# Optimization experiments

Measured on AMD Instinct MI355X. Metric: run time of the kernel, lower is better.

Reference implementation:

```python
import jax, jax.numpy as jnp
import numpy as np

B, LP, LQ, D = 32, 2048, 512, 256

def setup_inputs() -> dict:
    key = jax.random.key(0)
    k1, k2, k3, k4 = jax.random.split(key, 4)
    x = jax.random.normal(k1, (B, LP, D), dtype=jnp.float32)
    y = jax.random.normal(k2, (B, LQ, D), dtype=jnp.float32)
    # nn.Linear(input_size, input_size): weight [D, D], bias [D]
    bound = 1.0 / np.sqrt(D)
    W = jax.random.uniform(k3, (D, D), minval=-bound, maxval=bound, dtype=jnp.float32)
    b = jax.random.uniform(k4, (D,), minval=-bound, maxval=bound, dtype=jnp.float32)
    return {"x": x, "y": y, "W": W, "b": b}

def reference(x, y, W, b):
    # shared linear + relu projection (torch Linear: x @ W.T + b)
    x_proj = jax.nn.relu(jnp.einsum('bpd,ed->bpe', x, W) + b)  # [B, LP, D]
    y_proj = jax.nn.relu(jnp.einsum('bqd,ed->bqe', y, W) + b)  # [B, LQ, D]
    # unscaled cross-attention scores
    scores = jnp.einsum('bpd,bqd->bpq', x_proj, y_proj)        # [B, LP, LQ]
    alpha = jax.nn.softmax(scores, axis=-1)
    # weighted sum over original (unprojected) y
    match_seq = jnp.einsum('bpq,bqd->bpd', alpha, y)           # [B, LP, D]
    return match_seq
```

## Files before the change

kernel.cpp:

```cpp
#include <hip/hip_runtime.h>
#include <stdint.h>

#define B_  32
#define LP_ 2048
#define LQ_ 512
#define D_  256

typedef __attribute__((ext_vector_type(8))) short short8;
typedef __attribute__((ext_vector_type(8))) _Float16 f16x8;
typedef __attribute__((ext_vector_type(4))) float f32x4;

__device__ __forceinline__ ushort f2h(float x) {
    union { _Float16 h; ushort u; } v;
    v.h = (_Float16)x;
    return v.u;
}
__device__ __forceinline__ void gl_lds16(const void* g, void* l) {
    __builtin_amdgcn_global_load_lds(
        (const __attribute__((address_space(1))) void*)g,
        (__attribute__((address_space(3))) void*)l, 16, 0, 0);
}


__global__ void k_prep(const float* __restrict__ W, const float* __restrict__ y,
                       ushort* __restrict__ Whf, ushort* __restrict__ yf) {
    __shared__ float t[32 * 260];
    if (blockIdx.x < 256) {
        int i = blockIdx.x * 256 + threadIdx.x;
        int e = i >> 8, k = i & 255;
        size_t off = (size_t)((k >> 5) * 16 + (e >> 4)) * 512 +
                     ((k >> 3) & 3) * 128 + (e & 15) * 8 + (k & 7);
        Whf[off] = f2h(W[i]);
        return;
    }
    int bid = blockIdx.x - 256;
    int b = bid >> 4, qc = bid & 15;
    int tid = threadIdx.x;
    int ql = tid >> 3;
    int d0 = (tid & 7) * 4;
#pragma unroll
    for (int p = 0; p < 8; p++) {
        int d = p * 32 + d0;
        float4 v = *(const float4*)(y + ((size_t)(b * LQ_ + qc * 32 + ql) * 256 + d));
        t[ql * 260 + d + 0] = v.x; t[ql * 260 + d + 1] = v.y;
        t[ql * 260 + d + 2] = v.z; t[ql * 260 + d + 3] = v.w;
    }
    __syncthreads();
    int w = tid >> 6, L = tid & 63, c = L & 15, quad = L >> 4;
#pragma unroll
    for (int ii = 0; ii < 4; ii++) {
        int nt = w * 4 + ii;
        short8 o;
#pragma unroll
        for (int j = 0; j < 8; j++)
            o[j] = (short)f2h(t[(quad * 8 + j) * 260 + nt * 16 + c]);
        *(short8*)(yf + ((size_t)(b * 256 + qc * 16 + nt) * 512 + L * 8)) = o;
    }
}

__global__ __launch_bounds__(256, 3) void k_proj(const float* __restrict__ y,
                                                 const ushort* __restrict__ Whf,
                                                 const float* __restrict__ bias,
                                                 ushort* __restrict__ Oy) {
    __shared__ __align__(16) ushort Ws[16704];
    const int tid  = threadIdx.x;
    const int w    = tid >> 6;
    const int L    = tid & 63;
    const int c    = L & 15;
    const int quad = L >> 4;
    const int row0 = blockIdx.x * 64 + w * 16;
    const int arow = row0 + c;

    f32x4 acc[16];
#pragma unroll
    for (int i = 0; i < 16; i++) acc[i] = (f32x4)0.f;

#define PSTAGE(kc, p)                                                          \
    {                                                                          \
        _Pragma("unroll")                                                      \
        for (int ii = 0; ii < 4; ii++) {                                       \
            int i = w * 4 + ii;                                                \
            gl_lds16(Whf + (size_t)(kc) * 8192 + i * 512 + L * 8,              \
                     (char*)Ws + (p) * 16384 + i * 1024);                      \
        }                                                                      \
    }

    PSTAGE(0, 0);
    float4 nx0 = *(const float4*)(y + (size_t)arow * 256 + quad * 8);
    float4 nx1 = *(const float4*)(y + (size_t)arow * 256 + quad * 8 + 4);

    for (int kc = 0; kc < 8; kc++) {
        __syncthreads();
        if (kc < 7) PSTAGE(kc + 1, (kc + 1) & 1);
        float4 cx0 = nx0, cx1 = nx1;
        if (kc < 7) {
            nx0 = *(const float4*)(y + (size_t)arow * 256 + (kc + 1) * 32 + quad * 8);
            nx1 = *(const float4*)(y + (size_t)arow * 256 + (kc + 1) * 32 + quad * 8 + 4);
        }
        float xs[8] = {cx0.x, cx0.y, cx0.z, cx0.w, cx1.x, cx1.y, cx1.z, cx1.w};
        f16x8 ah;
#pragma unroll
        for (int j = 0; j < 8; j++) ah[j] = (_Float16)xs[j];
        const ushort* buf = Ws + (kc & 1) * 8192;
#pragma unroll
        for (int nt = 0; nt < 16; nt++) {
            f16x8 bh = *(const f16x8*)(buf + nt * 512 + L * 8);
            acc[nt] = __builtin_amdgcn_mfma_f32_16x16x32_f16(ah, bh, acc[nt], 0, 0, 0);
        }
    }

    __syncthreads();
    float* tr = (float*)Ws + w * (16 * 130);
    const int rt_g = row0 >> 4;
#pragma unroll
    for (int half = 0; half < 2; half++) {
#pragma unroll
        for (int nt8 = 0; nt8 < 8; nt8++) {
            int nt = half * 8 + nt8;
            float bv = bias[nt * 16 + c];
#pragma unroll
            for (int r = 0; r < 4; r++)
                tr[(quad * 4 + r) * 130 + nt8 * 16 + c] = fmaxf(acc[nt][r] + bv, 0.f);
        }
#pragma unroll
        for (int ec4 = 0; ec4 < 4; ec4++) {
            int ec = half * 4 + ec4;
            short8 hh;
#pragma unroll
            for (int j = 0; j < 8; j++)
                hh[j] = (short)f2h(tr[c * 130 + ec4 * 32 + quad * 8 + j]);
            size_t blk = (size_t)(rt_g >> 5) * 256 + ec * 32 + (rt_g & 31);
            *(short8*)(Oy + blk * 512 + L * 8) = hh;
        }
    }
}

__global__ __launch_bounds__(256, 4) void k_attn(const float* __restrict__ x,
                                                 const ushort* __restrict__ Whf,
                                                 const float* __restrict__ bias,
                                                 const ushort* __restrict__ ypf,
                                                 const ushort* __restrict__ yf,
                                                 float* __restrict__ out) {
    __shared__ __align__(16) ushort lds[16384];
    const int tid  = threadIdx.x;
    const int w    = tid >> 6;
    const int L    = tid & 63;
    const int c    = L & 15;
    const int quad = L >> 4;

    const int bid = blockIdx.x;
    const int jj  = bid >> 3;
    const int b   = (bid & 7) * 4 + (jj >> 6);
    const int mt  = jj & 63;
    const int m0  = mt * 32;

#pragma unroll
    for (int ii = 0; ii < 4; ii++) {
        int unit = w * 4 + ii;
        int rs = unit >> 3, kc = unit & 7;
        const float* xs = x + ((size_t)(b * LP_ + m0 + rs * 16 + c)) * 256 + kc * 32 + quad * 8;
        float4 v0 = *(const float4*)xs;
        float4 v1 = *(const float4*)(xs + 4);
        f16x8 h;
        h[0] = (_Float16)v0.x; h[1] = (_Float16)v0.y;
        h[2] = (_Float16)v0.z; h[3] = (_Float16)v0.w;
        h[4] = (_Float16)v1.x; h[5] = (_Float16)v1.y;
        h[6] = (_Float16)v1.z; h[7] = (_Float16)v1.w;
        *(f16x8*)(lds + unit * 512 + L * 8) = h;
    }
    __syncthreads();

    {
        float bv[4];
#pragma unroll
        for (int ne = 0; ne < 4; ne++) bv[ne] = bias[(w * 4 + ne) * 16 + c];
        f32x4 pacc[2][4];
#pragma unroll
        for (int rs = 0; rs < 2; rs++)
#pragma unroll
            for (int ne = 0; ne < 4; ne++) pacc[rs][ne] = (f32x4)0.f;
        for (int kc = 0; kc < 8; kc++) {
            f16x8 ah0 = *(const f16x8*)(lds + kc * 512 + L * 8);
            f16x8 ah1 = *(const f16x8*)(lds + (8 + kc) * 512 + L * 8);
#pragma unroll
            for (int ne = 0; ne < 4; ne++) {
                f16x8 wb = *(const f16x8*)(Whf + ((size_t)(kc * 16 + w * 4 + ne)) * 512 + L * 8);
                pacc[0][ne] = __builtin_amdgcn_mfma_f32_16x16x32_f16(ah0, wb, pacc[0][ne], 0, 0, 0);
                pacc[1][ne] = __builtin_amdgcn_mfma_f32_16x16x32_f16(ah1, wb, pacc[1][ne], 0, 0, 0);
            }
        }
#pragma unroll
        for (int rs = 0; rs < 2; rs++)
#pragma unroll
            for (int ne = 0; ne < 4; ne++) {
#pragma unroll
                for (int r = 0; r < 4; r++) {
                    float v = fmaxf(pacc[rs][ne][r] + bv[ne], 0.f);
                    int off = 8192 + (rs * 8 + w * 2 + (ne >> 1)) * 512 +
                              ((ne & 1) * 2 + (c >> 3)) * 128 + (quad * 4 + r) * 8 + (c & 7);
                    lds[off] = f2h(v);
                }
            }
    }

    f32x4 sc[2][8];
#pragma unroll
    for (int rs = 0; rs < 2; rs++)
#pragma unroll
        for (int qt = 0; qt < 8; qt++) sc[rs][qt] = (f32x4)0.f;
    __syncthreads();

    const ushort* pf = lds + 8192;
    const ushort* yb = ypf + (size_t)b * 256 * 512;
    for (int kc = 0; kc < 8; kc++) {
        f16x8 ah0 = *(const f16x8*)(pf + kc * 512 + L * 8);
        f16x8 ah1 = *(const f16x8*)(pf + (8 + kc) * 512 + L * 8);
#pragma unroll
        for (int qt = 0; qt < 8; qt++) {
            f16x8 bh = *(const f16x8*)(yb + ((size_t)kc * 32 + w * 8 + qt) * 512 + L * 8);
            sc[0][qt] = __builtin_amdgcn_mfma_f32_16x16x32_f16(ah0, bh, sc[0][qt], 0, 0, 0);
            sc[1][qt] = __builtin_amdgcn_mfma_f32_16x16x32_f16(ah1, bh, sc[1][qt], 0, 0, 0);
        }
    }

    __syncthreads();
    float* red  = (float*)lds;
    float* red2 = red + 128;
    float inv[2][4];
#pragma unroll
    for (int rs = 0; rs < 2; rs++)
#pragma unroll
        for (int r = 0; r < 4; r++) {
            float pm = sc[rs][0][r];
#pragma unroll
            for (int qt = 1; qt < 8; qt++) pm = fmaxf(pm, sc[rs][qt][r]);
#pragma unroll
            for (int mask = 1; mask <= 8; mask <<= 1) pm = fmaxf(pm, __shfl_xor(pm, mask));
            if (c == 0) red[(rs * 16 + quad * 4 + r) * 4 + w] = pm;
        }
    __syncthreads();
#pragma unroll
    for (int rs = 0; rs < 2; rs++)
#pragma unroll
        for (int r = 0; r < 4; r++) {
            int row = rs * 16 + quad * 4 + r;
            float m = fmaxf(fmaxf(red[row * 4], red[row * 4 + 1]),
                            fmaxf(red[row * 4 + 2], red[row * 4 + 3]));
            float ps = 0.f;
#pragma unroll
            for (int qt = 0; qt < 8; qt++) {
                float e = __expf(sc[rs][qt][r] - m);
                sc[rs][qt][r] = e;
                ps += e;
            }
#pragma unroll
            for (int mask = 1; mask <= 8; mask <<= 1) ps += __shfl_xor(ps, mask);
            if (c == 0) red2[row * 4 + w] = ps;
        }
    __syncthreads();
#pragma unroll
    for (int rs = 0; rs < 2; rs++)
#pragma unroll
        for (int r = 0; r < 4; r++) {
            int row = rs * 16 + quad * 4 + r;
            inv[rs][r] = 1.f / (red2[row * 4] + red2[row * 4 + 1] +
                                red2[row * 4 + 2] + red2[row * 4 + 3]);
        }
    __syncthreads();

#pragma unroll
    for (int rs = 0; rs < 2; rs++)
#pragma unroll
        for (int r = 0; r < 4; r++) {
            int m_loc = rs * 16 + quad * 4 + r;
            int swz = m_loc & 7;
            float iv = inv[rs][r];
#pragma unroll
            for (int qt = 0; qt < 8; qt++) {
                int q = w * 128 + qt * 16 + c;
                lds[m_loc * 512 + (((q >> 3) ^ swz) << 3) + (c & 7)] = f2h(sc[rs][qt][r] * iv);
            }
        }
    __syncthreads();

    f32x4 o[2][4];
#pragma unroll
    for (int rs = 0; rs < 2; rs++)
#pragma unroll
        for (int dt = 0; dt < 4; dt++) o[rs][dt] = (f32x4)0.f;
    const int dh = w;
    const int swzA = c & 7;
    for (int kcq = 0; kcq < 16; kcq++) {
        int chunk = kcq * 4 + quad;
        f16x8 af0 = *(const f16x8*)(lds + c * 512 + ((chunk ^ swzA) << 3));
        f16x8 af1 = *(const f16x8*)(lds + (16 + c) * 512 + ((chunk ^ swzA) << 3));
        const ushort* ybf = yf + ((size_t)(b * 256 + kcq * 16 + dh * 4)) * 512;
#pragma unroll
        for (int dt = 0; dt < 4; dt++) {
            f16x8 bfr = *(const f16x8*)(ybf + dt * 512 + L * 8);
            o[0][dt] = __builtin_amdgcn_mfma_f32_16x16x32_f16(af0, bfr, o[0][dt], 0, 0, 0);
            o[1][dt] = __builtin_amdgcn_mfma_f32_16x16x32_f16(af1, bfr, o[1][dt], 0, 0, 0);
        }
    }

#pragma unroll
    for (int rs = 0; rs < 2; rs++)
#pragma unroll
        for (int dt = 0; dt < 4; dt++)
#pragma unroll
            for (int r = 0; r < 4; r++) {
                int row = rs * 16 + quad * 4 + r;
                out[(size_t)(b * LP_ + m0 + row) * 256 + dh * 64 + dt * 16 + c] =
                    o[rs][dt][r];
            }
}

extern "C" void kernel_launch(void* const* d_in, const int* in_sizes, int n_in,
                              void* d_out, int out_size, void* d_ws, size_t ws_size,
                              hipStream_t stream) {
    const float* x    = (const float*)d_in[0];
    const float* y    = (const float*)d_in[1];
    const float* W    = (const float*)d_in[2];
    const float* bias = (const float*)d_in[3];
    float* out = (float*)d_out;

    char* ws = (char*)d_ws;
    size_t off = 0;
    ushort* Whf = (ushort*)(ws + off); off += (size_t)D_ * D_ * 2;
    ushort* yfb = (ushort*)(ws + off); off += (size_t)B_ * D_ * LQ_ * 2;
    ushort* ypf = (ushort*)(ws + off); off += (size_t)B_ * LQ_ * D_ * 2;

    k_prep<<<768, 256, 0, stream>>>(W, y, Whf, yfb);
    k_proj<<<256, 256, 0, stream>>>(y, Whf, bias, ypf);
    k_attn<<<B_ * 64, 256, 0, stream>>>(x, Whf, bias, ypf, yfb, out);
}
```

Before: 196.4 us.

## Double-buffer W and projected-y fragments in LDS via async global-to-LDS loads

Weight fragments for the projection GEMM and projected-y fragments for the score GEMM are now staged into double-buffered LDS with global_load_lds. The next chunk is prefetched while MFMAs run on the current one, instead of each wave loading directly from global memory inside the MFMA loop. The score phase is also repartitioned so each wave owns one 16-row slab and half the q columns, which simplifies the softmax reductions to two partials per row. This raises LDS use to 48KB per block, which may cut occupancy below the 4 blocks per CU in launch bounds, and adds many more barriers.

```diff
diff --git a/kernel.cpp b/kernel.cpp
--- a/kernel.cpp
+++ b/kernel.cpp
@@ -141,7 +141,7 @@
                                                  const ushort* __restrict__ ypf,
                                                  const ushort* __restrict__ yf,
                                                  float* __restrict__ out) {
-    __shared__ __align__(16) ushort lds[16384];
+    __shared__ __align__(16) ushort lds[24576];
     const int tid  = threadIdx.x;
     const int w    = tid >> 6;
     const int L    = tid & 63;
@@ -168,7 +168,10 @@
         h[6] = (_Float16)v1.z; h[7] = (_Float16)v1.w;
         *(f16x8*)(lds + unit * 512 + L * 8) = h;
     }
-    __syncthreads();
+#pragma unroll
+    for (int ii = 0; ii < 4; ii++)
+        gl_lds16(Whf + (size_t)(w * 4 + ii) * 512 + L * 8,
+                 (char*)lds + 16384 + (w * 4 + ii) * 1024);
 
     {
         float bv[4];
@@ -179,16 +182,30 @@
         for (int rs = 0; rs < 2; rs++)
 #pragma unroll
             for (int ne = 0; ne < 4; ne++) pacc[rs][ne] = (f32x4)0.f;
+#pragma unroll
         for (int kc = 0; kc < 8; kc++) {
+            __syncthreads();
+            if (kc < 7) {
+#pragma unroll
+                for (int ii = 0; ii < 4; ii++)
+                    gl_lds16(Whf + (size_t)((kc + 1) * 16 + w * 4 + ii) * 512 + L * 8,
+                             (char*)lds + 16384 + ((kc + 1) & 1) * 16384 + (w * 4 + ii) * 1024);
+            }
             f16x8 ah0 = *(const f16x8*)(lds + kc * 512 + L * 8);
             f16x8 ah1 = *(const f16x8*)(lds + (8 + kc) * 512 + L * 8);
+            const ushort* wbuf = lds + 8192 + (kc & 1) * 8192;
 #pragma unroll
             for (int ne = 0; ne < 4; ne++) {
-                f16x8 wb = *(const f16x8*)(Whf + ((size_t)(kc * 16 + w * 4 + ne)) * 512 + L * 8);
+                f16x8 wb = *(const f16x8*)(wbuf + (w * 4 + ne) * 512 + L * 8);
                 pacc[0][ne] = __builtin_amdgcn_mfma_f32_16x16x32_f16(ah0, wb, pacc[0][ne], 0, 0, 0);
                 pacc[1][ne] = __builtin_amdgcn_mfma_f32_16x16x32_f16(ah1, wb, pacc[1][ne], 0, 0, 0);
             }
         }
+        __syncthreads();
+#pragma unroll
+        for (int ii = 0; ii < 4; ii++)
+            gl_lds16(ypf + ((size_t)b * 256 + (w * 4 + ii)) * 512 + L * 8,
+                     (char*)lds + 16384 + (w * 4 + ii) * 1024);
 #pragma unroll
         for (int rs = 0; rs < 2; rs++)
 #pragma unroll
@@ -196,91 +213,95 @@
 #pragma unroll
                 for (int r = 0; r < 4; r++) {
                     float v = fmaxf(pacc[rs][ne][r] + bv[ne], 0.f);
-                    int off = 8192 + (rs * 8 + w * 2 + (ne >> 1)) * 512 +
+                    int off = (rs * 8 + w * 2 + (ne >> 1)) * 512 +
                               ((ne & 1) * 2 + (c >> 3)) * 128 + (quad * 4 + r) * 8 + (c & 7);
                     lds[off] = f2h(v);
                 }
             }
     }
-
-    f32x4 sc[2][8];
-#pragma unroll
-    for (int rs = 0; rs < 2; rs++)
-#pragma unroll
-        for (int qt = 0; qt < 8; qt++) sc[rs][qt] = (f32x4)0.f;
-    __syncthreads();
-
-    const ushort* pf = lds + 8192;
-    const ushort* yb = ypf + (size_t)b * 256 * 512;
-    for (int kc = 0; kc < 8; kc++) {
-        f16x8 ah0 = *(const f16x8*)(pf + kc * 512 + L * 8);
-        f16x8 ah1 = *(const f16x8*)(pf + (8 + kc) * 512 + L * 8);
-#pragma unroll
-        for (int qt = 0; qt < 8; qt++) {
-            f16x8 bh = *(const f16x8*)(yb + ((size_t)kc * 32 + w * 8 + qt) * 512 + L * 8);
-            sc[0][qt] = __builtin_amdgcn_mfma_f32_16x16x32_f16(ah0, bh, sc[0][qt], 0, 0, 0);
-            sc[1][qt] = __builtin_amdgcn_mfma_f32_16x16x32_f16(ah1, bh, sc[1][qt], 0, 0, 0);
-        }
-    }
-
-    __syncthreads();
+    __syncthreads();
+
+    const int rsw = w & 1, ow = w >> 1;
+    f32x4 sc2[2][8];
+#pragma unroll
+    for (int qH = 0; qH < 2; qH++)
+#pragma unroll
+        for (int t = 0; t < 8; t++) sc2[qH][t] = (f32x4)0.f;
+#pragma unroll
+    for (int s = 0; s < 16; s++) {
+        if (s > 0) __syncthreads();
+        if (s < 15) {
+            int kcn = (s + 1) >> 1, qHn = (s + 1) & 1;
+#pragma unroll
+            for (int ii = 0; ii < 4; ii++)
+                gl_lds16(ypf + ((size_t)b * 256 + kcn * 32 + qHn * 16 + w * 4 + ii) * 512 + L * 8,
+                         (char*)lds + 16384 + ((s + 1) & 1) * 16384 + (w * 4 + ii) * 1024);
+        }
+        int kc = s >> 1, qH = s & 1;
+        f16x8 ah = *(const f16x8*)(lds + (rsw * 8 + kc) * 512 + L * 8);
+        const ushort* bbuf = lds + 8192 + (s & 1) * 8192;
+#pragma unroll
+        for (int t = 0; t < 8; t++) {
+            f16x8 bh = *(const f16x8*)(bbuf + (ow * 8 + t) * 512 + L * 8);
+            sc2[qH][t] = __builtin_amdgcn_mfma_f32_16x16x32_f16(ah, bh, sc2[qH][t], 0, 0, 0);
+        }
+    }
+    __syncthreads();
+
     float* red  = (float*)lds;
-    float* red2 = red + 128;
-    float inv[2][4];
-#pragma unroll
-    for (int rs = 0; rs < 2; rs++)
-#pragma unroll
-        for (int r = 0; r < 4; r++) {
-            float pm = sc[rs][0][r];
-#pragma unroll
-            for (int qt = 1; qt < 8; qt++) pm = fmaxf(pm, sc[rs][qt][r]);
-#pragma unroll
-            for (int mask = 1; mask <= 8; mask <<= 1) pm = fmaxf(pm, __shfl_xor(pm, mask));
-            if (c == 0) red[(rs * 16 + quad * 4 + r) * 4 + w] = pm;
-        }
-    __syncthreads();
-#pragma unroll
-    for (int rs = 0; rs < 2; rs++)
-#pragma unroll
-        for (int r = 0; r < 4; r++) {
-            int row = rs * 16 + quad * 4 + r;
-            float m = fmaxf(fmaxf(red[row * 4], red[row * 4 + 1]),
-                            fmaxf(red[row * 4 + 2], red[row * 4 + 3]));
-            float ps = 0.f;
-#pragma unroll
-            for (int qt = 0; qt < 8; qt++) {
-                float e = __expf(sc[rs][qt][r] - m);
-                sc[rs][qt][r] = e;
+    float* red2 = red + 64;
+    float inv[4];
+#pragma unroll
+    for (int r = 0; r < 4; r++) {
+        float pm = sc2[0][0][r];
+#pragma unroll
+        for (int qH = 0; qH < 2; qH++)
+#pragma unroll
+            for (int t = 0; t < 8; t++) pm = fmaxf(pm, sc2[qH][t][r]);
+#pragma unroll
+        for (int mask = 1; mask <= 8; mask <<= 1) pm = fmaxf(pm, __shfl_xor(pm, mask));
+        if (c == 0) red[(rsw * 16 + quad * 4 + r) * 2 + ow] = pm;
+    }
+    __syncthreads();
+#pragma unroll
+    for (int r = 0; r < 4; r++) {
+        int row = rsw * 16 + quad * 4 + r;
+        float m = fmaxf(red[row * 2], red[row * 2 + 1]);
+        float ps = 0.f;
+#pragma unroll
+        for (int qH = 0; qH < 2; qH++)
+#pragma unroll
+            for (int t = 0; t < 8; t++) {
+                float e = __expf(sc2[qH][t][r] - m);
+                sc2[qH][t][r] = e;
                 ps += e;
             }
 #pragma unroll
-            for (int mask = 1; mask <= 8; mask <<= 1) ps += __shfl_xor(ps, mask);
-            if (c == 0) red2[row * 4 + w] = ps;
-        }
-    __syncthreads();
-#pragma unroll
-    for (int rs = 0; rs < 2; rs++)
-#pragma unroll
-        for (int r = 0; r < 4; r++) {
-            int row = rs * 16 + quad * 4 + r;
-            inv[rs][r] = 1.f / (red2[row * 4] + red2[row * 4 + 1] +
-                                red2[row * 4 + 2] + red2[row * 4 + 3]);
-        }
-    __syncthreads();
-
-#pragma unroll
-    for (int rs = 0; rs < 2; rs++)
-#pragma unroll
-        for (int r = 0; r < 4; r++) {
-            int m_loc = rs * 16 + quad * 4 + r;
-            int swz = m_loc & 7;
-            float iv = inv[rs][r];
-#pragma unroll
-            for (int qt = 0; qt < 8; qt++) {
-                int q = w * 128 + qt * 16 + c;
-                lds[m_loc * 512 + (((q >> 3) ^ swz) << 3) + (c & 7)] = f2h(sc[rs][qt][r] * iv);
-            }
-        }
+        for (int mask = 1; mask <= 8; mask <<= 1) ps += __shfl_xor(ps, mask);
+        if (c == 0) red2[row * 2 + ow] = ps;
+    }
+    __syncthreads();
+#pragma unroll
+    for (int r = 0; r < 4; r++) {
+        int row = rsw * 16 + quad * 4 + r;
+        inv[r] = 1.f / (red2[row * 2] + red2[row * 2 + 1]);
+    }
+    __syncthreads();
+
+#pragma unroll
+    for (int r = 0; r < 4; r++) {
+        int m_loc = rsw * 16 + quad * 4 + r;
+        int swz = m_loc & 7;
+        float iv = inv[r];
+#pragma unroll
+        for (int qH = 0; qH < 2; qH++)
+#pragma unroll
+            for (int t = 0; t < 8; t++) {
+                int q = (qH * 16 + ow * 8 + t) * 16 + c;
+                lds[8192 + m_loc * 512 + (((q >> 3) ^ swz) << 3) + (c & 7)] =
+                    f2h(sc2[qH][t][r] * iv);
+            }
+    }
     __syncthreads();
 
     f32x4 o[2][4];
@@ -292,8 +313,8 @@
     const int swzA = c & 7;
     for (int kcq = 0; kcq < 16; kcq++) {
         int chunk = kcq * 4 + quad;
-        f16x8 af0 = *(const f16x8*)(lds + c * 512 + ((chunk ^ swzA) << 3));
-        f16x8 af1 = *(const f16x8*)(lds + (16 + c) * 512 + ((chunk ^ swzA) << 3));
+        f16x8 af0 = *(const f16x8*)(lds + 8192 + c * 512 + ((chunk ^ swzA) << 3));
+        f16x8 af1 = *(const f16x8*)(lds + 8192 + (16 + c) * 512 + ((chunk ^ swzA) << 3));
         const ushort* ybf = yf + ((size_t)(b * 256 + kcq * 16 + dh * 4)) * 512;
 #pragma unroll
         for (int dt = 0; dt < 4; dt++) {
```

Result: slower. 206.4 us (+5.1%).

## Stream y operands through LDS with double-buffered async global-to-LDS loads

Applied to the files above, without the earlier changes.

The scores and output GEMM loops in k_attn now prefetch the ypf and yf fragments into per-wave LDS double buffers using global_load_lds, instead of loading them straight into registers from global memory each iteration. Explicit vmcnt/lgkmcnt waits overlap the next chunk's fetch with the current MFMAs. LDS grows from 32KB to 48KB and launch bounds drop from 4 to 3 blocks per CU, giving up some occupancy in exchange for hidden load latency.

```diff
diff --git a/kernel.cpp b/kernel.cpp
--- a/kernel.cpp
+++ b/kernel.cpp
@@ -135,13 +135,13 @@
     }
 }
 
-__global__ __launch_bounds__(256, 4) void k_attn(const float* __restrict__ x,
+__global__ __launch_bounds__(256, 3) void k_attn(const float* __restrict__ x,
                                                  const ushort* __restrict__ Whf,
                                                  const float* __restrict__ bias,
                                                  const ushort* __restrict__ ypf,
                                                  const ushort* __restrict__ yf,
                                                  float* __restrict__ out) {
-    __shared__ __align__(16) ushort lds[16384];
+    __shared__ __align__(16) ushort lds[24576];
     const int tid  = threadIdx.x;
     const int w    = tid >> 6;
     const int L    = tid & 63;
@@ -210,17 +210,44 @@
         for (int qt = 0; qt < 8; qt++) sc[rs][qt] = (f32x4)0.f;
     __syncthreads();
 
-    const ushort* pf = lds + 8192;
-    const ushort* yb = ypf + (size_t)b * 256 * 512;
-    for (int kc = 0; kc < 8; kc++) {
-        f16x8 ah0 = *(const f16x8*)(pf + kc * 512 + L * 8);
-        f16x8 ah1 = *(const f16x8*)(pf + (8 + kc) * 512 + L * 8);
-#pragma unroll
-        for (int qt = 0; qt < 8; qt++) {
-            f16x8 bh = *(const f16x8*)(yb + ((size_t)kc * 32 + w * 8 + qt) * 512 + L * 8);
-            sc[0][qt] = __builtin_amdgcn_mfma_f32_16x16x32_f16(ah0, bh, sc[0][qt], 0, 0, 0);
-            sc[1][qt] = __builtin_amdgcn_mfma_f32_16x16x32_f16(ah1, bh, sc[1][qt], 0, 0, 0);
-        }
+    asm volatile("s_waitcnt vmcnt(0)" ::: "memory");
+    const int abase = (w & 1) * 4096 + (w >> 1) * 16384;
+#pragma unroll
+    for (int i = 0; i < 4; i++)
+        gl_lds16(ypf + ((size_t)b * 256 + w * 8 + i) * 512 + L * 8,
+                 (char*)lds + (size_t)(abase + i * 512) * 2);
+#pragma unroll
+    for (int i = 0; i < 4; i++)
+        gl_lds16(ypf + ((size_t)b * 256 + w * 8 + 4 + i) * 512 + L * 8,
+                 (char*)lds + (size_t)(abase + 2048 + i * 512) * 2);
+#pragma unroll
+    for (int s = 0; s < 16; s++) {
+        if (s < 15) { asm volatile("s_waitcnt vmcnt(4)" ::: "memory"); }
+        else        { asm volatile("s_waitcnt vmcnt(0)" ::: "memory"); }
+        const int kc = s >> 1, qhf = s & 1;
+        const ushort* sb = lds + abase + (s & 1) * 2048;
+        f16x8 ah0 = *(const f16x8*)(lds + 8192 + kc * 512 + L * 8);
+        f16x8 ah1 = *(const f16x8*)(lds + 8192 + (8 + kc) * 512 + L * 8);
+        f16x8 bh0 = *(const f16x8*)(sb + 0 * 512 + L * 8);
+        f16x8 bh1 = *(const f16x8*)(sb + 1 * 512 + L * 8);
+        f16x8 bh2 = *(const f16x8*)(sb + 2 * 512 + L * 8);
+        f16x8 bh3 = *(const f16x8*)(sb + 3 * 512 + L * 8);
+        asm volatile("s_waitcnt lgkmcnt(0)" ::: "memory");
+        if (s < 14) {
+            const int kn = (s + 2) >> 1, qn = (s + 2) & 1;
+#pragma unroll
+            for (int i = 0; i < 4; i++)
+                gl_lds16(ypf + ((size_t)b * 256 + kn * 32 + w * 8 + qn * 4 + i) * 512 + L * 8,
+                         (char*)lds + (size_t)(abase + (s & 1) * 2048 + i * 512) * 2);
+        }
+        sc[0][qhf * 4 + 0] = __builtin_amdgcn_mfma_f32_16x16x32_f16(ah0, bh0, sc[0][qhf * 4 + 0], 0, 0, 0);
+        sc[1][qhf * 4 + 0] = __builtin_amdgcn_mfma_f32_16x16x32_f16(ah1, bh0, sc[1][qhf * 4 + 0], 0, 0, 0);
+        sc[0][qhf * 4 + 1] = __builtin_amdgcn_mfma_f32_16x16x32_f16(ah0, bh1, sc[0][qhf * 4 + 1], 0, 0, 0);
+        sc[1][qhf * 4 + 1] = __builtin_amdgcn_mfma_f32_16x16x32_f16(ah1, bh1, sc[1][qhf * 4 + 1], 0, 0, 0);
+        sc[0][qhf * 4 + 2] = __builtin_amdgcn_mfma_f32_16x16x32_f16(ah0, bh2, sc[0][qhf * 4 + 2], 0, 0, 0);
+        sc[1][qhf * 4 + 2] = __builtin_amdgcn_mfma_f32_16x16x32_f16(ah1, bh2, sc[1][qhf * 4 + 2], 0, 0, 0);
+        sc[0][qhf * 4 + 3] = __builtin_amdgcn_mfma_f32_16x16x32_f16(ah0, bh3, sc[0][qhf * 4 + 3], 0, 0, 0);
+        sc[1][qhf * 4 + 3] = __builtin_amdgcn_mfma_f32_16x16x32_f16(ah1, bh3, sc[1][qhf * 4 + 3], 0, 0, 0);
     }
 
     __syncthreads();
@@ -288,19 +315,40 @@
     for (int rs = 0; rs < 2; rs++)
 #pragma unroll
         for (int dt = 0; dt < 4; dt++) o[rs][dt] = (f32x4)0.f;
-    const int dh = w;
     const int swzA = c & 7;
-    for (int kcq = 0; kcq < 16; kcq++) {
-        int chunk = kcq * 4 + quad;
+    asm volatile("s_waitcnt vmcnt(0)" ::: "memory");
+    const int cbase = 16384 + w * 2048;
+#pragma unroll
+    for (int i = 0; i < 2; i++)
+        gl_lds16(yf + ((size_t)(b * 256 + w * 4 + i)) * 512 + L * 8,
+                 (char*)lds + (size_t)(cbase + i * 512) * 2);
+#pragma unroll
+    for (int i = 0; i < 2; i++)
+        gl_lds16(yf + ((size_t)(b * 256 + w * 4 + 2 + i)) * 512 + L * 8,
+                 (char*)lds + (size_t)(cbase + 1024 + i * 512) * 2);
+#pragma unroll
+    for (int s = 0; s < 32; s++) {
+        if (s < 31) { asm volatile("s_waitcnt vmcnt(2)" ::: "memory"); }
+        else        { asm volatile("s_waitcnt vmcnt(0)" ::: "memory"); }
+        const int kcq = s >> 1, dp = s & 1;
+        const ushort* sb = lds + cbase + (s & 1) * 1024;
+        const int chunk = kcq * 4 + quad;
         f16x8 af0 = *(const f16x8*)(lds + c * 512 + ((chunk ^ swzA) << 3));
         f16x8 af1 = *(const f16x8*)(lds + (16 + c) * 512 + ((chunk ^ swzA) << 3));
-        const ushort* ybf = yf + ((size_t)(b * 256 + kcq * 16 + dh * 4)) * 512;
-#pragma unroll
-        for (int dt = 0; dt < 4; dt++) {
-            f16x8 bfr = *(const f16x8*)(ybf + dt * 512 + L * 8);
-            o[0][dt] = __builtin_amdgcn_mfma_f32_16x16x32_f16(af0, bfr, o[0][dt], 0, 0, 0);
-            o[1][dt] = __builtin_amdgcn_mfma_f32_16x16x32_f16(af1, bfr, o[1][dt], 0, 0, 0);
-        }
+        f16x8 bf0 = *(const f16x8*)(sb + L * 8);
+        f16x8 bf1 = *(const f16x8*)(sb + 512 + L * 8);
+        asm volatile("s_waitcnt lgkmcnt(0)" ::: "memory");
+        if (s < 30) {
+            const int kn = (s + 2) >> 1, dn = (s + 2) & 1;
+#pragma unroll
+            for (int i = 0; i < 2; i++)
+                gl_lds16(yf + ((size_t)(b * 256 + kn * 16 + w * 4 + dn * 2 + i)) * 512 + L * 8,
+                         (char*)lds + (size_t)(cbase + (s & 1) * 1024 + i * 512) * 2);
+        }
+        o[0][dp * 2 + 0] = __builtin_amdgcn_mfma_f32_16x16x32_f16(af0, bf0, o[0][dp * 2 + 0], 0, 0, 0);
+        o[1][dp * 2 + 0] = __builtin_amdgcn_mfma_f32_16x16x32_f16(af1, bf0, o[1][dp * 2 + 0], 0, 0, 0);
+        o[0][dp * 2 + 1] = __builtin_amdgcn_mfma_f32_16x16x32_f16(af0, bf1, o[0][dp * 2 + 1], 0, 0, 0);
+        o[1][dp * 2 + 1] = __builtin_amdgcn_mfma_f32_16x16x32_f16(af1, bf1, o[1][dp * 2 + 1], 0, 0, 0);
     }
 
 #pragma unroll
@@ -310,7 +358,7 @@
 #pragma unroll
             for (int r = 0; r < 4; r++) {
                 int row = rs * 16 + quad * 4 + r;
-                out[(size_t)(b * LP_ + m0 + row) * 256 + dh * 64 + dt * 16 + c] =
+                out[(size_t)(b * LP_ + m0 + row) * 256 + w * 64 + dt * 16 + c] =
                     o[rs][dt][r];
             }
 }
```

Result: slower. 204.3 us (+4.0%).

## Double attention row tile to 64 and merge softmax max/sum passes

Applied to the files above, without the earlier changes.

Each attention block now handles 64 query rows instead of 32, so every global load of W, projected y and y fragments feeds four row tiles rather than two. Per-block LDS doubles and launch bounds drop to two blocks per CU. The softmax now computes wave-local max and sum in one pass and rescales with an online-softmax style correction, which removes one reduction round and two barriers. Each thread holds more accumulators, which raises register pressure and lowers occupancy, and the grid has half as many blocks.

```diff
diff --git a/kernel.cpp b/kernel.cpp
--- a/kernel.cpp
+++ b/kernel.cpp
@@ -135,13 +135,13 @@
     }
 }
 
-__global__ __launch_bounds__(256, 4) void k_attn(const float* __restrict__ x,
+__global__ __launch_bounds__(256, 2) void k_attn(const float* __restrict__ x,
                                                  const ushort* __restrict__ Whf,
                                                  const float* __restrict__ bias,
                                                  const ushort* __restrict__ ypf,
                                                  const ushort* __restrict__ yf,
                                                  float* __restrict__ out) {
-    __shared__ __align__(16) ushort lds[16384];
+    __shared__ __align__(16) ushort lds[32768];
     const int tid  = threadIdx.x;
     const int w    = tid >> 6;
     const int L    = tid & 63;
@@ -150,15 +150,15 @@
 
     const int bid = blockIdx.x;
     const int jj  = bid >> 3;
-    const int b   = (bid & 7) * 4 + (jj >> 6);
-    const int mt  = jj & 63;
-    const int m0  = mt * 32;
-
-#pragma unroll
-    for (int ii = 0; ii < 4; ii++) {
-        int unit = w * 4 + ii;
-        int rs = unit >> 3, kc = unit & 7;
-        const float* xs = x + ((size_t)(b * LP_ + m0 + rs * 16 + c)) * 256 + kc * 32 + quad * 8;
+    const int b   = (bid & 7) * 4 + (jj >> 5);
+    const int mt  = jj & 31;
+    const int m0  = mt * 64;
+
+#pragma unroll
+    for (int ii = 0; ii < 8; ii++) {
+        int unit = w * 8 + ii;
+        int rt = unit >> 3, kc = unit & 7;
+        const float* xs = x + ((size_t)(b * LP_ + m0 + rt * 16 + c)) * 256 + kc * 32 + quad * 8;
         float4 v0 = *(const float4*)xs;
         float4 v1 = *(const float4*)(xs + 4);
         f16x8 h;
@@ -174,144 +174,151 @@
         float bv[4];
 #pragma unroll
         for (int ne = 0; ne < 4; ne++) bv[ne] = bias[(w * 4 + ne) * 16 + c];
-        f32x4 pacc[2][4];
-#pragma unroll
-        for (int rs = 0; rs < 2; rs++)
-#pragma unroll
-            for (int ne = 0; ne < 4; ne++) pacc[rs][ne] = (f32x4)0.f;
+        f32x4 pacc[4][4];
+#pragma unroll
+        for (int rt = 0; rt < 4; rt++)
+#pragma unroll
+            for (int ne = 0; ne < 4; ne++) pacc[rt][ne] = (f32x4)0.f;
         for (int kc = 0; kc < 8; kc++) {
-            f16x8 ah0 = *(const f16x8*)(lds + kc * 512 + L * 8);
-            f16x8 ah1 = *(const f16x8*)(lds + (8 + kc) * 512 + L * 8);
+            f16x8 wb[4];
+#pragma unroll
+            for (int ne = 0; ne < 4; ne++)
+                wb[ne] = *(const f16x8*)(Whf + ((size_t)(kc * 16 + w * 4 + ne)) * 512 + L * 8);
+#pragma unroll
+            for (int rt = 0; rt < 4; rt++) {
+                f16x8 ah = *(const f16x8*)(lds + (rt * 8 + kc) * 512 + L * 8);
+#pragma unroll
+                for (int ne = 0; ne < 4; ne++)
+                    pacc[rt][ne] = __builtin_amdgcn_mfma_f32_16x16x32_f16(ah, wb[ne], pacc[rt][ne], 0, 0, 0);
+            }
+        }
+#pragma unroll
+        for (int rt = 0; rt < 4; rt++)
 #pragma unroll
             for (int ne = 0; ne < 4; ne++) {
-                f16x8 wb = *(const f16x8*)(Whf + ((size_t)(kc * 16 + w * 4 + ne)) * 512 + L * 8);
-                pacc[0][ne] = __builtin_amdgcn_mfma_f32_16x16x32_f16(ah0, wb, pacc[0][ne], 0, 0, 0);
-                pacc[1][ne] = __builtin_amdgcn_mfma_f32_16x16x32_f16(ah1, wb, pacc[1][ne], 0, 0, 0);
-            }
-        }
-#pragma unroll
-        for (int rs = 0; rs < 2; rs++)
-#pragma unroll
-            for (int ne = 0; ne < 4; ne++) {
 #pragma unroll
                 for (int r = 0; r < 4; r++) {
-                    float v = fmaxf(pacc[rs][ne][r] + bv[ne], 0.f);
-                    int off = 8192 + (rs * 8 + w * 2 + (ne >> 1)) * 512 +
+                    float v = fmaxf(pacc[rt][ne][r] + bv[ne], 0.f);
+                    int off = 16384 + (rt * 8 + w * 2 + (ne >> 1)) * 512 +
                               ((ne & 1) * 2 + (c >> 3)) * 128 + (quad * 4 + r) * 8 + (c & 7);
                     lds[off] = f2h(v);
                 }
             }
     }
 
-    f32x4 sc[2][8];
-#pragma unroll
-    for (int rs = 0; rs < 2; rs++)
-#pragma unroll
-        for (int qt = 0; qt < 8; qt++) sc[rs][qt] = (f32x4)0.f;
-    __syncthreads();
-
-    const ushort* pf = lds + 8192;
+    f32x4 sc[4][8];
+#pragma unroll
+    for (int rt = 0; rt < 4; rt++)
+#pragma unroll
+        for (int qt = 0; qt < 8; qt++) sc[rt][qt] = (f32x4)0.f;
+    __syncthreads();
+
+    const ushort* pf = lds + 16384;
     const ushort* yb = ypf + (size_t)b * 256 * 512;
     for (int kc = 0; kc < 8; kc++) {
-        f16x8 ah0 = *(const f16x8*)(pf + kc * 512 + L * 8);
-        f16x8 ah1 = *(const f16x8*)(pf + (8 + kc) * 512 + L * 8);
+        f16x8 ah[4];
+#pragma unroll
+        for (int rt = 0; rt < 4; rt++)
+            ah[rt] = *(const f16x8*)(pf + (rt * 8 + kc) * 512 + L * 8);
 #pragma unroll
         for (int qt = 0; qt < 8; qt++) {
             f16x8 bh = *(const f16x8*)(yb + ((size_t)kc * 32 + w * 8 + qt) * 512 + L * 8);
-            sc[0][qt] = __builtin_amdgcn_mfma_f32_16x16x32_f16(ah0, bh, sc[0][qt], 0, 0, 0);
-            sc[1][qt] = __builtin_amdgcn_mfma_f32_16x16x32_f16(ah1, bh, sc[1][qt], 0, 0, 0);
-        }
-    }
-
-    __syncthreads();
+#pragma unroll
+            for (int rt = 0; rt < 4; rt++)
+                sc[rt][qt] = __builtin_amdgcn_mfma_f32_16x16x32_f16(ah[rt], bh, sc[rt][qt], 0, 0, 0);
+        }
+    }
+
     float* red  = (float*)lds;
-    float* red2 = red + 128;
-    float inv[2][4];
-#pragma unroll
-    for (int rs = 0; rs < 2; rs++)
+    float* red2 = red + 256;
+    float pmv[4][4], scl[4][4];
+#pragma unroll
+    for (int rt = 0; rt < 4; rt++)
 #pragma unroll
         for (int r = 0; r < 4; r++) {
-            float pm = sc[rs][0][r];
-#pragma unroll
-            for (int qt = 1; qt < 8; qt++) pm = fmaxf(pm, sc[rs][qt][r]);
+            float pm = sc[rt][0][r];
+#pragma unroll
+            for (int qt = 1; qt < 8; qt++) pm = fmaxf(pm, sc[rt][qt][r]);
 #pragma unroll
             for (int mask = 1; mask <= 8; mask <<= 1) pm = fmaxf(pm, __shfl_xor(pm, mask));
-            if (c == 0) red[(rs * 16 + quad * 4 + r) * 4 + w] = pm;
-        }
-    __syncthreads();
-#pragma unroll
-    for (int rs = 0; rs < 2; rs++)
+            float ps = 0.f;
+#pragma unroll
+            for (int qt = 0; qt < 8; qt++) {
+                float e = __expf(sc[rt][qt][r] - pm);
+                sc[rt][qt][r] = e;
+                ps += e;
+            }
+#pragma unroll
+            for (int mask = 1; mask <= 8; mask <<= 1) ps += __shfl_xor(ps, mask);
+            pmv[rt][r] = pm;
+            if (c == 0) {
+                int row = rt * 16 + quad * 4 + r;
+                red[row * 4 + w]  = pm;
+                red2[row * 4 + w] = ps;
+            }
+        }
+    __syncthreads();
+#pragma unroll
+    for (int rt = 0; rt < 4; rt++)
 #pragma unroll
         for (int r = 0; r < 4; r++) {
-            int row = rs * 16 + quad * 4 + r;
-            float m = fmaxf(fmaxf(red[row * 4], red[row * 4 + 1]),
-                            fmaxf(red[row * 4 + 2], red[row * 4 + 3]));
-            float ps = 0.f;
-#pragma unroll
-            for (int qt = 0; qt < 8; qt++) {
-                float e = __expf(sc[rs][qt][r] - m);
-                sc[rs][qt][r] = e;
-                ps += e;
-            }
-#pragma unroll
-            for (int mask = 1; mask <= 8; mask <<= 1) ps += __shfl_xor(ps, mask);
-            if (c == 0) red2[row * 4 + w] = ps;
-        }
-    __syncthreads();
-#pragma unroll
-    for (int rs = 0; rs < 2; rs++)
+            int row = rt * 16 + quad * 4 + r;
+            float m0f = fmaxf(fmaxf(red[row * 4], red[row * 4 + 1]),
+                              fmaxf(red[row * 4 + 2], red[row * 4 + 3]));
+            float S = red2[row * 4] * __expf(red[row * 4] - m0f)
+                    + red2[row * 4 + 1] * __expf(red[row * 4 + 1] - m0f)
+                    + red2[row * 4 + 2] * __expf(red[row * 4 + 2] - m0f)
+                    + red2[row * 4 + 3] * __expf(red[row * 4 + 3] - m0f);
+            scl[rt][r] = __expf(pmv[rt][r] - m0f) / S;
+        }
+    __syncthreads();
+
+#pragma unroll
+    for (int rt = 0; rt < 4; rt++)
 #pragma unroll
         for (int r = 0; r < 4; r++) {
-            int row = rs * 16 + quad * 4 + r;
-            inv[rs][r] = 1.f / (red2[row * 4] + red2[row * 4 + 1] +
-                                red2[row * 4 + 2] + red2[row * 4 + 3]);
-        }
-    __syncthreads();
-
-#pragma unroll
-    for (int rs = 0; rs < 2; rs++)
-#pragma unroll
-        for (int r = 0; r < 4; r++) {
-            int m_loc = rs * 16 + quad * 4 + r;
+            int m_loc = rt * 16 + quad * 4 + r;
             int swz = m_loc & 7;
-            float iv = inv[rs][r];
+            float iv = scl[rt][r];
 #pragma unroll
             for (int qt = 0; qt < 8; qt++) {
                 int q = w * 128 + qt * 16 + c;
-                lds[m_loc * 512 + (((q >> 3) ^ swz) << 3) + (c & 7)] = f2h(sc[rs][qt][r] * iv);
-            }
-        }
-    __syncthreads();
-
-    f32x4 o[2][4];
-#pragma unroll
-    for (int rs = 0; rs < 2; rs++)
-#pragma unroll
-        for (int dt = 0; dt < 4; dt++) o[rs][dt] = (f32x4)0.f;
-    const int dh = w;
+                lds[m_loc * 512 + (((q >> 3) ^ swz) << 3) + (c & 7)] = f2h(sc[rt][qt][r] * iv);
+            }
+        }
+    __syncthreads();
+
+    f32x4 o[4][4];
+#pragma unroll
+    for (int rt = 0; rt < 4; rt++)
+#pragma unroll
+        for (int dt = 0; dt < 4; dt++) o[rt][dt] = (f32x4)0.f;
     const int swzA = c & 7;
     for (int kcq = 0; kcq < 16; kcq++) {
         int chunk = kcq * 4 + quad;
-        f16x8 af0 = *(const f16x8*)(lds + c * 512 + ((chunk ^ swzA) << 3));
-        f16x8 af1 = *(const f16x8*)(lds + (16 + c) * 512 + ((chunk ^ swzA) << 3));
-        const ushort* ybf = yf + ((size_t)(b * 256 + kcq * 16 + dh * 4)) * 512;
+        f16x8 af[4];
+#pragma unroll
+        for (int rt = 0; rt < 4; rt++)
+            af[rt] = *(const f16x8*)(lds + (rt * 16 + c) * 512 + ((chunk ^ swzA) << 3));
+        const ushort* ybf = yf + ((size_t)(b * 256 + kcq * 16 + w * 4)) * 512;
 #pragma unroll
         for (int dt = 0; dt < 4; dt++) {
             f16x8 bfr = *(const f16x8*)(ybf + dt * 512 + L * 8);
-            o[0][dt] = __builtin_amdgcn_mfma_f32_16x16x32_f16(af0, bfr, o[0][dt], 0, 0, 0);
-            o[1][dt] = __builtin_amdgcn_mfma_f32_16x16x32_f16(af1, bfr, o[1][dt], 0, 0, 0);
-        }
-    }
-
-#pragma unroll
-    for (int rs = 0; rs < 2; rs++)
+#pragma unroll
+            for (int rt = 0; rt < 4; rt++)
+                o[rt][dt] = __builtin_amdgcn_mfma_f32_16x16x32_f16(af[rt], bfr, o[rt][dt], 0, 0, 0);
+        }
+    }
+
+#pragma unroll
+    for (int rt = 0; rt < 4; rt++)
 #pragma unroll
         for (int dt = 0; dt < 4; dt++)
 #pragma unroll
             for (int r = 0; r < 4; r++) {
-                int row = rs * 16 + quad * 4 + r;
-                out[(size_t)(b * LP_ + m0 + row) * 256 + dh * 64 + dt * 16 + c] =
-                    o[rs][dt][r];
+                int row = rt * 16 + quad * 4 + r;
+                out[(size_t)(b * LP_ + m0 + row) * 256 + w * 64 + dt * 16 + c] =
+                    o[rt][dt][r];
             }
 }
 
@@ -332,5 +339,5 @@
 
     k_prep<<<768, 256, 0, stream>>>(W, y, Whf, yfb);
     k_proj<<<256, 256, 0, stream>>>(y, Whf, bias, ypf);
-    k_attn<<<B_ * 64, 256, 0, stream>>>(x, Whf, bias, ypf, yfb, out);
-}
+    k_attn<<<B_ * 32, 256, 0, stream>>>(x, Whf, bias, ypf, yfb, out);
+}
```

After: 208.2 us. +6.0%, slower.
